# Performance work log

Hardware: AMD Instinct MI355X
Metric: run time of the kernel (lower is better)

Reference implementation:

```python
import jax, jax.numpy as jnp
import numpy as np

B, S, D, H, DK = 8, 1024, 1024, 16, 64
DV = D // H  # 64


def setup_inputs() -> dict:
    key = jax.random.key(0)
    ks = jax.random.split(key, 9)
    s = 1.0 / np.sqrt(D)
    return {
        "x": jax.random.normal(ks[0], (B, S, D), dtype=jnp.float32),
        "masks": jnp.ones((B, S), dtype=jnp.int32),
        "Wq": jax.random.normal(ks[1], (D, H * DK), dtype=jnp.float32) * s,
        "bq": jnp.zeros((H * DK,), dtype=jnp.float32),
        "Wk": jax.random.normal(ks[2], (D, H * DK), dtype=jnp.float32) * s,
        "bk": jnp.zeros((H * DK,), dtype=jnp.float32),
        "Wv": jax.random.normal(ks[3], (D, H * DV), dtype=jnp.float32) * s,
        "bv": jnp.zeros((H * DV,), dtype=jnp.float32),
        "Wo": jax.random.normal(ks[4], (H * DV, D), dtype=jnp.float32) * s,
        "bo": jnpp_zeros() if False else jnp.zeros((D,), dtype=jnp.float32),
    }


def reference(x, masks, Wq, bq, Wk, bk, Wv, bv, Wo, bo):
    # projections -> [B, H, S, d]
    q = (x @ Wq + bq).reshape(B, S, H, DK).transpose(0, 2, 1, 3)
    k = (x @ Wk + bk).reshape(B, S, H, DK).transpose(0, 2, 1, 3)
    v = (x @ Wv + bv).reshape(B, S, H, DV).transpose(0, 2, 1, 3)
    # scaled dot-product attention with padding mask
    logits = jnp.einsum('bhqd,bhkd->bhqk', q, k) / jnp.sqrt(jnp.float32(DK))
    mask = masks[:, None, None, :]  # [B,1,1,S]
    logits = jnp.where(mask == 0, jnp.float32(-1e9), logits)
    scores = jax.nn.softmax(logits, axis=-1)
    out = jnp.einsum('bhqk,bhkd->bhqd', scores, v)
    out = out.transpose(0, 2, 1, 3).reshape(B, S, H * DV)
    # output projection; dropout is identity in eval mode
    return out @ Wo + bo
```

## Files before the change

kernel.cpp:

```cpp
#include <hip/hip_runtime.h>
#include <stdint.h>

#define B_ 8
#define S_ 1024
#define D_ 1024
#define H_ 16
#define DK_ 64
#define DV_ 64

typedef __attribute__((ext_vector_type(8))) short short8;
typedef __attribute__((ext_vector_type(4))) float f32x4;

__device__ __forceinline__ unsigned short f2bf(float f) {
  union { float f; unsigned u; } v; v.f = f;
  return (unsigned short)((v.u + 0x7fffu + ((v.u >> 16) & 1u)) >> 16);
}
__device__ __forceinline__ unsigned short f2bf_trunc(float f) {
  union { float f; unsigned u; } v; v.f = f;
  return (unsigned short)(v.u >> 16);
}

__device__ __forceinline__ void ld_lds16(const unsigned short* g, unsigned short* l) {
  __builtin_amdgcn_global_load_lds((const __attribute__((address_space(1))) void*)g,
                                   (__attribute__((address_space(3))) void*)l, 16, 0, 0);
}

__global__ __launch_bounds__(256) void prep_kernel(const float* __restrict__ x,
                                                   unsigned short* __restrict__ xb,
                                                   const float* __restrict__ W0,
                                                   const float* __restrict__ W1,
                                                   const float* __restrict__ W2,
                                                   const float* __restrict__ W3,
                                                   unsigned short* __restrict__ T0,
                                                   unsigned short* __restrict__ T1,
                                                   unsigned short* __restrict__ T2,
                                                   unsigned short* __restrict__ T3) {
  const int z = blockIdx.z;
  if (z >= 4) {
    size_t blk = (size_t)(z - 4) * 256 + blockIdx.y * 16 + blockIdx.x;
    size_t i = (blk * 256 + threadIdx.x) * 4;
    float4 v = *(const float4*)(x + i);
    ushort4 o;
    o.x = f2bf(v.x); o.y = f2bf(v.y); o.z = f2bf(v.z); o.w = f2bf(v.w);
    *(ushort4*)(xb + i) = o;
    return;
  }
  __shared__ __align__(16) unsigned short tl[64][65];
  const float* W; unsigned short* Wt;
  switch (z) {
    case 0: W = W0; Wt = T0; break;
    case 1: W = W1; Wt = T1; break;
    case 2: W = W2; Wt = T2; break;
    default: W = W3; Wt = T3; break;
  }
  const int xx = threadIdx.x & 63;
  const int y4 = threadIdx.x >> 6;
  const int bn = blockIdx.x * 64;
  const int bk = blockIdx.y * 64;
  #pragma unroll
  for (int r = y4; r < 64; r += 4)
    tl[r][xx] = f2bf(W[(size_t)(bk + r) * 1024 + bn + xx]);
  __syncthreads();
  #pragma unroll
  for (int r = y4; r < 64; r += 4)
    Wt[(size_t)(bn + r) * 1024 + bk + xx] = tl[xx][r];
}

__device__ __forceinline__ void stage_tile64(const unsigned short* __restrict__ G,
                                             unsigned short* __restrict__ Ls,
                                             int t, int wslot, size_t rowstride, int k0) {
  #pragma unroll
  for (int i = 0; i < 4; i++) {
    int s = i * 256 + t;
    int r = s >> 3, c = (s & 7) ^ (r & 7);
    ld_lds16(G + (size_t)r * rowstride + k0 + c * 8, &Ls[(i * 256 + wslot) * 8]);
  }
}

__global__ __launch_bounds__(256) void gemm_qkv(const unsigned short* __restrict__ A,
                                                const unsigned short* __restrict__ Bt,
                                                const float* __restrict__ bq,
                                                const float* __restrict__ bk,
                                                const float* __restrict__ bv,
                                                const int* __restrict__ masks,
                                                unsigned short* __restrict__ q,
                                                unsigned short* __restrict__ kk,
                                                unsigned short* __restrict__ vT) {
  const int K = 1024;
  __shared__ __align__(16) unsigned short As[128 * 64];
  __shared__ __align__(16) unsigned short Bs[128 * 64];
  const int t = threadIdx.x;
  const int wave = t >> 6, lane = t & 63;
  const int l15 = lane & 15, quad = lane >> 4;
  const int l7 = l15 & 7;
  const int bm = blockIdx.y * 128, bn = blockIdx.x * 128;
  const int wm = (wave & 1) * 64, wn = (wave >> 1) * 64;
  const bool vsec = (blockIdx.x >= 16);
  const int wslot = (t & ~63);

  f32x4 acc[4][4] = {};
  const unsigned short* Ag = A + (size_t)bm * K;
  const unsigned short* Bg = Bt + (size_t)bn * K;

  for (int k0 = 0; k0 < K; k0 += 64) {
    __syncthreads();
    stage_tile64(Ag, As, t, wslot, K, k0);
    stage_tile64(Bg, Bs, t, wslot, K, k0);
    __syncthreads();
    #pragma unroll
    for (int kf = 0; kf < 2; kf++) {
      short8 af[4], bf[4];
      #pragma unroll
      for (int mi = 0; mi < 4; mi++)
        af[mi] = *(const short8*)&As[(wm + mi * 16 + l15) * 64 + (((kf << 2) | quad) ^ l7) * 8];
      #pragma unroll
      for (int ni = 0; ni < 4; ni++)
        bf[ni] = *(const short8*)&Bs[(wn + ni * 16 + l15) * 64 + (((kf << 2) | quad) ^ l7) * 8];
      if (vsec) {
        #pragma unroll
        for (int mi = 0; mi < 4; mi++)
          #pragma unroll
          for (int ni = 0; ni < 4; ni++)
            acc[mi][ni] = __builtin_amdgcn_mfma_f32_16x16x32_bf16(bf[ni], af[mi], acc[mi][ni], 0, 0, 0);
      } else {
        #pragma unroll
        for (int mi = 0; mi < 4; mi++)
          #pragma unroll
          for (int ni = 0; ni < 4; ni++)
            acc[mi][ni] = __builtin_amdgcn_mfma_f32_16x16x32_bf16(af[mi], bf[ni], acc[mi][ni], 0, 0, 0);
      }
    }
  }

  if (!vsec) {
    int sec = blockIdx.x >> 3;
    const float* bsel = (sec == 0) ? bq : bk;
    unsigned short* dst = (sec == 0) ? q : kk;
    float scale = (sec == 0) ? 0.180336880f : 1.0f;
    #pragma unroll
    for (int ni = 0; ni < 4; ni++) {
      int c = ((bn & 1023) + wn + ni * 16 + l15);
      float bvv = bsel[c];
      int hh = c >> 6, d = c & 63;
      #pragma unroll
      for (int mi = 0; mi < 4; mi++) {
        int row0 = bm + wm + mi * 16 + quad * 4;
        #pragma unroll
        for (int r = 0; r < 4; r++) {
          int row = row0 + r;
          int b = row >> 10, s = row & 1023;
          dst[(((size_t)(b * H_ + hh)) * S_ + s) * DK_ + d] = f2bf((acc[mi][ni][r] + bvv) * scale);
        }
      }
    }
  } else {
    #pragma unroll
    for (int ni = 0; ni < 4; ni++) {
      int cbase = (bn & 1023) + wn + ni * 16;
      #pragma unroll
      for (int mi = 0; mi < 4; mi++) {
        int row = bm + wm + mi * 16 + l15;
        int b = row >> 10, s = row & 1023;
        float mf = (masks[b * S_ + s] != 0) ? 1.0f : 0.0f;
        #pragma unroll
        for (int r = 0; r < 4; r++) {
          int c = cbase + quad * 4 + r;
          int hh = c >> 6, d = c & 63;
          vT[(((size_t)(b * H_ + hh)) * DV_ + d) * S_ + s] = f2bf((acc[mi][ni][r] + bv[c]) * mf);
        }
      }
    }
  }
}

__global__ __launch_bounds__(256) void gemm_out(const unsigned short* __restrict__ A,
                                                const unsigned short* __restrict__ Bt,
                                                const float* __restrict__ bias,
                                                float* __restrict__ Cout) {
  const int K = 1024, N = 1024;
  __shared__ __align__(16) unsigned short As[128 * 64];
  __shared__ __align__(16) unsigned short Bs[128 * 64];
  const int t = threadIdx.x;
  const int wave = t >> 6, lane = t & 63;
  const int l15 = lane & 15, quad = lane >> 4;
  const int l7 = l15 & 7;
  const int bm = blockIdx.y * 128, bn = blockIdx.x * 128;
  const int wm = (wave & 1) * 64, wn = (wave >> 1) * 64;
  const int wslot = (t & ~63);

  f32x4 acc[4][4] = {};
  const unsigned short* Ag = A + (size_t)bm * K;
  const unsigned short* Bg = Bt + (size_t)bn * K;

  for (int k0 = 0; k0 < K; k0 += 64) {
    __syncthreads();
    stage_tile64(Ag, As, t, wslot, K, k0);
    stage_tile64(Bg, Bs, t, wslot, K, k0);
    __syncthreads();
    #pragma unroll
    for (int kf = 0; kf < 2; kf++) {
      short8 af[4], bf[4];
      #pragma unroll
      for (int mi = 0; mi < 4; mi++)
        af[mi] = *(const short8*)&As[(wm + mi * 16 + l15) * 64 + (((kf << 2) | quad) ^ l7) * 8];
      #pragma unroll
      for (int ni = 0; ni < 4; ni++)
        bf[ni] = *(const short8*)&Bs[(wn + ni * 16 + l15) * 64 + (((kf << 2) | quad) ^ l7) * 8];
      #pragma unroll
      for (int mi = 0; mi < 4; mi++)
        #pragma unroll
        for (int ni = 0; ni < 4; ni++)
          acc[mi][ni] = __builtin_amdgcn_mfma_f32_16x16x32_bf16(af[mi], bf[ni], acc[mi][ni], 0, 0, 0);
    }
  }

  #pragma unroll
  for (int ni = 0; ni < 4; ni++) {
    int col = bn + wn + ni * 16 + l15;
    float bvv = bias[col];
    #pragma unroll
    for (int mi = 0; mi < 4; mi++) {
      int row0 = bm + wm + mi * 16 + quad * 4;
      #pragma unroll
      for (int r = 0; r < 4; r++)
        Cout[(size_t)(row0 + r) * N + col] = acc[mi][ni][r] + bvv;
    }
  }
}

#define PLD 72
__global__ __launch_bounds__(256) void attn_kernel(const unsigned short* __restrict__ Q,
                                                   const unsigned short* __restrict__ Kb,
                                                   const unsigned short* __restrict__ Vt,
                                                   const int* __restrict__ masks,
                                                   unsigned short* __restrict__ O) {
  __shared__ __align__(16) unsigned short QP[128 * PLD];
  __shared__ __align__(16) unsigned short Ks[64 * 64];
  __shared__ __align__(16) unsigned short Vs[80 * 64];
  const int t = threadIdx.x;
  const int wave = t >> 6, lane = t & 63;
  const int l15 = lane & 15, quad = lane >> 4;
  const int l7 = l15 & 7;
  const int bh = blockIdx.x;
  const int qt = blockIdx.y;
  const int b = bh >> 4, h = bh & 15;

  const unsigned short* Qg = Q + ((size_t)bh * S_ + qt * 128) * DK_;
  const unsigned short* Kg = Kb + (size_t)bh * S_ * DK_;
  const unsigned short* Vg = Vt + (size_t)bh * DV_ * S_;
  const int wslot = (t & ~63);

  #pragma unroll
  for (int i = 0; i < 4; i++) {
    int p = i * 256 + t;
    ld_lds16(Qg + (size_t)p * 8, &QP[(i * 256 + wslot) * 8]);
  }
  __syncthreads();

  short8 aq[2][2];
  #pragma unroll
  for (int mb = 0; mb < 2; mb++)
    #pragma unroll
    for (int kf = 0; kf < 2; kf++)
      aq[mb][kf] = *(const short8*)&QP[(wave * 32 + mb * 16 + l15) * 64 + kf * 32 + quad * 8];

  f32x4 o_acc[2][5] = {};

  for (int kt = 0; kt < 16; kt++) {
    __syncthreads();
    #pragma unroll
    for (int i = 0; i < 2; i++) {
      int p = i * 256 + t;
      int rk = p >> 3, ck = (p & 7) ^ (rk & 7);
      ld_lds16(Kg + ((size_t)(kt * 64 + rk)) * DK_ + ck * 8, &Ks[(i * 256 + wslot) * 8]);
      ld_lds16(Vg + (size_t)rk * S_ + kt * 64 + ck * 8, &Vs[(i * 256 + wslot) * 8]);
    }
    if (wave == 0)
      Vs[64 * 64 + lane] = (masks[b * S_ + kt * 64 + lane] != 0) ? (unsigned short)0x3F80 : (unsigned short)0;
    __syncthreads();

    f32x4 sc[2][4];
    #pragma unroll
    for (int n = 0; n < 4; n++) {
      short8 bk0 = *(const short8*)&Ks[(n * 16 + l15) * 64 + (quad ^ l7) * 8];
      short8 bk1 = *(const short8*)&Ks[(n * 16 + l15) * 64 + ((4 + quad) ^ l7) * 8];
      #pragma unroll
      for (int mb = 0; mb < 2; mb++) {
        f32x4 c = {};
        c = __builtin_amdgcn_mfma_f32_16x16x32_bf16(bk0, aq[mb][0], c, 0, 0, 0);
        c = __builtin_amdgcn_mfma_f32_16x16x32_bf16(bk1, aq[mb][1], c, 0, 0, 0);
        sc[mb][n] = c;
      }
    }
    #pragma unroll
    for (int mb = 0; mb < 2; mb++)
      #pragma unroll
      for (int n = 0; n < 4; n++) {
        ushort4 pk;
        pk.x = f2bf_trunc(exp2f(sc[mb][n][0]));
        pk.y = f2bf_trunc(exp2f(sc[mb][n][1]));
        pk.z = f2bf_trunc(exp2f(sc[mb][n][2]));
        pk.w = f2bf_trunc(exp2f(sc[mb][n][3]));
        *(ushort4*)&QP[(wave * 32 + mb * 16 + l15) * PLD + n * 16 + quad * 4] = pk;
      }
    #pragma unroll
    for (int kf = 0; kf < 2; kf++) {
      short8 ap[2];
      #pragma unroll
      for (int mb = 0; mb < 2; mb++)
        ap[mb] = *(const short8*)&QP[(wave * 32 + mb * 16 + l15) * PLD + kf * 32 + quad * 8];
      #pragma unroll
      for (int n = 0; n < 5; n++) {
        short8 bv = *(const short8*)&Vs[(n * 16 + l15) * 64 + ((kf * 4 + quad) ^ l7) * 8];
        #pragma unroll
        for (int mb = 0; mb < 2; mb++)
          o_acc[mb][n] = __builtin_amdgcn_mfma_f32_16x16x32_bf16(ap[mb], bv, o_acc[mb][n], 0, 0, 0);
      }
    }
  }

  #pragma unroll
  for (int mb = 0; mb < 2; mb++)
    #pragma unroll
    for (int r = 0; r < 4; r++) {
      float l = __shfl(o_acc[mb][4][r], lane & 48, 64);
      float inv = 1.0f / l;
      int qrow = qt * 128 + wave * 32 + mb * 16 + quad * 4 + r;
      #pragma unroll
      for (int n = 0; n < 4; n++) {
        int col = h * 64 + n * 16 + l15;
        O[((size_t)b * S_ + qrow) * D_ + col] = f2bf(o_acc[mb][n][r] * inv);
      }
    }
}

extern "C" void kernel_launch(void* const* d_in, const int* in_sizes, int n_in,
                              void* d_out, int out_size, void* d_ws, size_t ws_size,
                              hipStream_t stream) {
  (void)in_sizes; (void)n_in; (void)out_size; (void)ws_size;
  const float* x  = (const float*)d_in[0];
  const int* masks = (const int*)d_in[1];
  const float* Wq = (const float*)d_in[2];
  const float* bq = (const float*)d_in[3];
  const float* Wk = (const float*)d_in[4];
  const float* bk = (const float*)d_in[5];
  const float* Wv = (const float*)d_in[6];
  const float* bv = (const float*)d_in[7];
  const float* Wo = (const float*)d_in[8];
  const float* bo = (const float*)d_in[9];

  char* p = (char*)d_ws;
  unsigned short* xb    = (unsigned short*)p; p += (size_t)8192 * 1024 * 2;
  unsigned short* WqkvT = (unsigned short*)p; p += (size_t)3072 * 1024 * 2;
  unsigned short* WoT   = (unsigned short*)p; p += (size_t)1024 * 1024 * 2;
  unsigned short* q     = (unsigned short*)p; p += (size_t)8192 * 1024 * 2;
  unsigned short* kk    = (unsigned short*)p; p += (size_t)8192 * 1024 * 2;
  unsigned short* vT    = (unsigned short*)p; p += (size_t)8192 * 1024 * 2;
  unsigned short* at    = (unsigned short*)p; p += (size_t)8192 * 1024 * 2;

  prep_kernel<<<dim3(16, 16, 36), 256, 0, stream>>>(
      x, xb, Wq, Wk, Wv, Wo,
      WqkvT, WqkvT + (size_t)1024 * 1024, WqkvT + (size_t)2048 * 1024, WoT);
  gemm_qkv<<<dim3(24, 64), 256, 0, stream>>>(xb, WqkvT, bq, bk, bv, masks, q, kk, vT);
  attn_kernel<<<dim3(128, 8), 256, 0, stream>>>(q, kk, vT, masks, at);
  gemm_out<<<dim3(8, 64), 256, 0, stream>>>(at, WoT, bo, (float*)d_out);
}
```

Before: 249.6 us.

## Register-prefetch next K/V tile to overlap global loads with attention compute

The attention loop used to issue direct global-to-LDS loads for each K/V tile and then wait on them. It now loads the next tile into registers while the current tile's MFMAs run, and stores them to LDS at the start of the following iteration. Mask values are also preloaded once into registers. This hides global load latency behind compute, at the cost of more VGPRs (possibly lower occupancy) and an extra LDS store pass through registers.

Measured after the change: 249.4 us. About the same (-0.1%).

```diff
diff --git a/kernel.cpp b/kernel.cpp
--- a/kernel.cpp
+++ b/kernel.cpp
@@ -255,6 +255,25 @@
     int p = i * 256 + t;
     ld_lds16(Qg + (size_t)p * 8, &QP[(i * 256 + wslot) * 8]);
   }
+
+  const int p0 = t, p1 = 256 + t;
+  const int rk0 = p0 >> 3, ck0 = (p0 & 7) ^ (rk0 & 7);
+  const int rk1 = p1 >> 3, ck1 = (p1 & 7) ^ (rk1 & 7);
+  const unsigned short* kp0 = Kg + (size_t)rk0 * DK_ + ck0 * 8;
+  const unsigned short* kp1 = Kg + (size_t)rk1 * DK_ + ck1 * 8;
+  const unsigned short* vp0 = Vg + (size_t)rk0 * S_ + ck0 * 8;
+  const unsigned short* vp1 = Vg + (size_t)rk1 * S_ + ck1 * 8;
+
+  int mv[4];
+  #pragma unroll
+  for (int j = 0; j < 4; j++)
+    mv[j] = masks[b * S_ + (j * 4 + wave) * 64 + lane];
+
+  short8 kr0 = *(const short8*)kp0;
+  short8 kr1 = *(const short8*)kp1;
+  short8 vr0 = *(const short8*)vp0;
+  short8 vr1 = *(const short8*)vp1;
+
   __syncthreads();
 
   short8 aq[2][2];
@@ -267,17 +286,21 @@
   f32x4 o_acc[2][5] = {};
 
   for (int kt = 0; kt < 16; kt++) {
-    __syncthreads();
-    #pragma unroll
-    for (int i = 0; i < 2; i++) {
-      int p = i * 256 + t;
-      int rk = p >> 3, ck = (p & 7) ^ (rk & 7);
-      ld_lds16(Kg + ((size_t)(kt * 64 + rk)) * DK_ + ck * 8, &Ks[(i * 256 + wslot) * 8]);
-      ld_lds16(Vg + (size_t)rk * S_ + kt * 64 + ck * 8, &Vs[(i * 256 + wslot) * 8]);
-    }
-    if (wave == 0)
-      Vs[64 * 64 + lane] = (masks[b * S_ + kt * 64 + lane] != 0) ? (unsigned short)0x3F80 : (unsigned short)0;
-    __syncthreads();
+    *(short8*)&Ks[p0 * 8] = kr0;
+    *(short8*)&Ks[p1 * 8] = kr1;
+    *(short8*)&Vs[p0 * 8] = vr0;
+    *(short8*)&Vs[p1 * 8] = vr1;
+    if (wave == (kt & 3))
+      Vs[64 * 64 + lane] = (mv[kt >> 2] != 0) ? (unsigned short)0x3F80 : (unsigned short)0;
+    __syncthreads();
+
+    if (kt < 15) {
+      kp0 += 64 * DK_; kp1 += 64 * DK_; vp0 += 64; vp1 += 64;
+      kr0 = *(const short8*)kp0;
+      kr1 = *(const short8*)kp1;
+      vr0 = *(const short8*)vp0;
+      vr1 = *(const short8*)vp1;
+    }
 
     f32x4 sc[2][4];
     #pragma unroll
@@ -317,6 +340,7 @@
           o_acc[mb][n] = __builtin_amdgcn_mfma_f32_16x16x32_bf16(ap[mb], bv, o_acc[mb][n], 0, 0, 0);
       }
     }
+    __syncthreads();
   }
 
   #pragma unroll
```

## Double-buffer K/V tiles in attention and use hardware exp2/rcp intrinsics

Applied to the files above, without the earlier changes.

The attention kernel now double-buffers the K and V tiles in LDS. It prefetches tile kt+1 while computing on tile kt and needs one barrier per iteration instead of two. Q fragments are loaded straight from global memory into registers rather than through LDS, and mask values are preloaded into registers once. exp2f and the final divide are swapped for the raw hardware exp2 and rcp intrinsics, trading some precision for fewer instructions; the doubled LDS footprint may lower occupancy.

Result: faster. 241.4 us (-3.3%).

```diff
diff --git a/kernel.cpp b/kernel.cpp
--- a/kernel.cpp
+++ b/kernel.cpp
@@ -229,14 +229,15 @@
 }
 
 #define PLD 72
+#define VROWS 65
 __global__ __launch_bounds__(256) void attn_kernel(const unsigned short* __restrict__ Q,
                                                    const unsigned short* __restrict__ Kb,
                                                    const unsigned short* __restrict__ Vt,
                                                    const int* __restrict__ masks,
                                                    unsigned short* __restrict__ O) {
-  __shared__ __align__(16) unsigned short QP[128 * PLD];
-  __shared__ __align__(16) unsigned short Ks[64 * 64];
-  __shared__ __align__(16) unsigned short Vs[80 * 64];
+  __shared__ __align__(16) unsigned short Pl[128 * PLD];
+  __shared__ __align__(16) unsigned short Ks[2 * 64 * 64];
+  __shared__ __align__(16) unsigned short Vs[(2 * VROWS + 15) * 64];
   const int t = threadIdx.x;
   const int wave = t >> 6, lane = t & 63;
   const int l15 = lane & 15, quad = lane >> 4;
@@ -250,40 +251,50 @@
   const unsigned short* Vg = Vt + (size_t)bh * DV_ * S_;
   const int wslot = (t & ~63);
 
-  #pragma unroll
-  for (int i = 0; i < 4; i++) {
-    int p = i * 256 + t;
-    ld_lds16(Qg + (size_t)p * 8, &QP[(i * 256 + wslot) * 8]);
-  }
-  __syncthreads();
+  int mv[4];
+  #pragma unroll
+  for (int j = 0; j < 4; j++)
+    mv[j] = masks[b * S_ + (j * 4 + wave) * 64 + lane];
 
   short8 aq[2][2];
   #pragma unroll
   for (int mb = 0; mb < 2; mb++)
     #pragma unroll
     for (int kf = 0; kf < 2; kf++)
-      aq[mb][kf] = *(const short8*)&QP[(wave * 32 + mb * 16 + l15) * 64 + kf * 32 + quad * 8];
-
-  f32x4 o_acc[2][5] = {};
-
-  for (int kt = 0; kt < 16; kt++) {
-    __syncthreads();
+      aq[mb][kf] = *(const short8*)(Qg + (size_t)(wave * 32 + mb * 16 + l15) * 64 + kf * 32 + quad * 8);
+
+  auto stage = [&](int kt, int buf) {
+    const unsigned short* Kt = Kg + (size_t)kt * 64 * DK_;
+    unsigned short* Kd = &Ks[buf * 4096];
+    unsigned short* Vd = &Vs[buf * (VROWS * 64)];
     #pragma unroll
     for (int i = 0; i < 2; i++) {
       int p = i * 256 + t;
       int rk = p >> 3, ck = (p & 7) ^ (rk & 7);
-      ld_lds16(Kg + ((size_t)(kt * 64 + rk)) * DK_ + ck * 8, &Ks[(i * 256 + wslot) * 8]);
-      ld_lds16(Vg + (size_t)rk * S_ + kt * 64 + ck * 8, &Vs[(i * 256 + wslot) * 8]);
-    }
-    if (wave == 0)
-      Vs[64 * 64 + lane] = (masks[b * S_ + kt * 64 + lane] != 0) ? (unsigned short)0x3F80 : (unsigned short)0;
-    __syncthreads();
+      ld_lds16(Kt + (size_t)rk * DK_ + ck * 8, &Kd[(i * 256 + wslot) * 8]);
+      ld_lds16(Vg + (size_t)rk * S_ + kt * 64 + ck * 8, &Vd[(i * 256 + wslot) * 8]);
+    }
+    if (wave == (kt & 3))
+      Vd[64 * 64 + lane] = (mv[kt >> 2] != 0) ? (unsigned short)0x3F80 : (unsigned short)0;
+  };
+
+  f32x4 o_acc[2][5] = {};
+
+  stage(0, 0);
+  __syncthreads();
+
+  #pragma unroll 2
+  for (int kt = 0; kt < 16; kt++) {
+    const int cur = kt & 1;
+    if (kt < 15) stage(kt + 1, cur ^ 1);
+    const unsigned short* Kc = &Ks[cur * 4096];
+    const unsigned short* Vc = &Vs[cur * (VROWS * 64)];
 
     f32x4 sc[2][4];
     #pragma unroll
     for (int n = 0; n < 4; n++) {
-      short8 bk0 = *(const short8*)&Ks[(n * 16 + l15) * 64 + (quad ^ l7) * 8];
-      short8 bk1 = *(const short8*)&Ks[(n * 16 + l15) * 64 + ((4 + quad) ^ l7) * 8];
+      short8 bk0 = *(const short8*)&Kc[(n * 16 + l15) * 64 + (quad ^ l7) * 8];
+      short8 bk1 = *(const short8*)&Kc[(n * 16 + l15) * 64 + ((4 + quad) ^ l7) * 8];
       #pragma unroll
       for (int mb = 0; mb < 2; mb++) {
         f32x4 c = {};
@@ -297,26 +308,27 @@
       #pragma unroll
       for (int n = 0; n < 4; n++) {
         ushort4 pk;
-        pk.x = f2bf_trunc(exp2f(sc[mb][n][0]));
-        pk.y = f2bf_trunc(exp2f(sc[mb][n][1]));
-        pk.z = f2bf_trunc(exp2f(sc[mb][n][2]));
-        pk.w = f2bf_trunc(exp2f(sc[mb][n][3]));
-        *(ushort4*)&QP[(wave * 32 + mb * 16 + l15) * PLD + n * 16 + quad * 4] = pk;
+        pk.x = f2bf_trunc(__builtin_amdgcn_exp2f(sc[mb][n][0]));
+        pk.y = f2bf_trunc(__builtin_amdgcn_exp2f(sc[mb][n][1]));
+        pk.z = f2bf_trunc(__builtin_amdgcn_exp2f(sc[mb][n][2]));
+        pk.w = f2bf_trunc(__builtin_amdgcn_exp2f(sc[mb][n][3]));
+        *(ushort4*)&Pl[(wave * 32 + mb * 16 + l15) * PLD + n * 16 + quad * 4] = pk;
       }
     #pragma unroll
     for (int kf = 0; kf < 2; kf++) {
       short8 ap[2];
       #pragma unroll
       for (int mb = 0; mb < 2; mb++)
-        ap[mb] = *(const short8*)&QP[(wave * 32 + mb * 16 + l15) * PLD + kf * 32 + quad * 8];
+        ap[mb] = *(const short8*)&Pl[(wave * 32 + mb * 16 + l15) * PLD + kf * 32 + quad * 8];
       #pragma unroll
       for (int n = 0; n < 5; n++) {
-        short8 bv = *(const short8*)&Vs[(n * 16 + l15) * 64 + ((kf * 4 + quad) ^ l7) * 8];
+        short8 bv = *(const short8*)&Vc[(n * 16 + l15) * 64 + ((kf * 4 + quad) ^ l7) * 8];
         #pragma unroll
         for (int mb = 0; mb < 2; mb++)
           o_acc[mb][n] = __builtin_amdgcn_mfma_f32_16x16x32_bf16(ap[mb], bv, o_acc[mb][n], 0, 0, 0);
       }
     }
+    __syncthreads();
   }
 
   #pragma unroll
@@ -324,7 +336,7 @@
     #pragma unroll
     for (int r = 0; r < 4; r++) {
       float l = __shfl(o_acc[mb][4][r], lane & 48, 64);
-      float inv = 1.0f / l;
+      float inv = __builtin_amdgcn_rcpf(l);
       int qrow = qt * 128 + wave * 32 + mb * 16 + quad * 4 + r;
       #pragma unroll
       for (int n = 0; n < 4; n++) {
```
